# Optimization experiments

Hardware: AMD Instinct MI355X
Metric: run time of the kernel (lower is better)

## Reference

```python
import math
import jax, jax.numpy as jnp
import numpy as np

P_NEW = 10000  # module init: new=10000


def _design_filter(p_full=10000, q_full=48000, L=10, beta=5.0):
    """Octave-style anti-alias FIR: kaiser-windowed sinc, normalized to sum 1
    (the module stores window = h / sum(h))."""
    g = math.gcd(p_full, q_full)
    p, q = p_full // g, q_full // g          # 5, 24
    order = 2 * L * max(p, q)                # 480 -> 481 taps (odd)
    t = np.arange(-order // 2, order // 2 + 1)
    cutoff = 1.0 / (2 * max(p, q))           # normalized cycles/sample
    h = 2 * cutoff * np.sinc(2 * cutoff * t) * np.kaiser(order + 1, beta)
    h = h / np.sum(h)
    return h.astype(np.float32)


def setup_inputs() -> dict:
    key = jax.random.key(0)
    B, T = 32, 1440000  # 32 channels, 30 s @ 48 kHz
    x = jax.random.normal(key, (B, T), dtype=jnp.float32)
    h = jnp.asarray(_design_filter())  # [481]
    return {"x": x, "h": h, "orig_fs": 48000}


def reference(x, h, orig_fs):
    # resample_poly: upsample by `up` (zero-insert), FIR filter, decimate by `down`
    up, down = P_NEW, int(orig_fs)
    g = math.gcd(up, down)
    up //= g
    down //= g                                   # 5, 24 for 48 kHz
    if up == 1 and down == 1:
        return x

    half_len = (h.shape[0] - 1) // 2
    h = h * up                                   # gain compensation
    n_in = x.shape[-1]

    n_pre_pad = (down - half_len % down) % down
    h_padded = jnp.pad(h, (n_pre_pad, 0))
    filt_len = h_padded.shape[0]
    h_flipped = jnp.flip(h_padded)[None, None, :]  # OIH

    x_flat = x.reshape(-1, 1, n_in)                # NCH
    # lhs_dilation=up == zero-stuffed upsample; torch pads filt_len-1 both sides
    # and the torch x_up carries (up-1) trailing zeros -> extra right pad.
    # window_strides=down == the y[..., ::down] decimation, computed without waste.
    y_down = jax.lax.conv_general_dilated(
        x_flat, h_flipped,
        window_strides=(down,),
        padding=[(filt_len - 1, filt_len - 1 + up - 1)],
        lhs_dilation=(up,),
        dimension_numbers=("NCH", "OIH", "NCH"),
    )

    n_out = n_in * up // down + (1 if (n_in * up) % down else 0)
    n_pre_remove = (half_len + n_pre_pad) // down
    y = y_down[..., n_pre_remove:n_pre_remove + n_out]
    return y.reshape(x.shape[:-1] + (n_out,))
```

## Files before the change

### kernel.cpp

```cpp
#include <hip/hip_runtime.h>


#define NIN    1440000
#define NOUTR  300000
#define NROWS  32
#define KTOT   60000
#define NCHUNK 938
#define S      8
#define NBX    118
#define TILE_E 1632
#define TILE_P 1648
#define NV4    408

typedef __attribute__((ext_vector_type(8))) short short8v;
typedef __attribute__((ext_vector_type(4))) float float4v;

__device__ __forceinline__ unsigned short f2b(float f) {
    unsigned u = __builtin_bit_cast(unsigned, f);
    u += 0x7fff + ((u >> 16) & 1);
    return (unsigned short)(u >> 16);
}

__global__ void prep_taps_kernel(const float* __restrict__ h,
                                 unsigned short* __restrict__ Bpk) {
    int i = blockIdx.x * blockDim.x + threadIdx.x;
    if (i < 2048) {
        int j = i & 7, l = (i >> 3) & 63, m = i >> 9;
        int d = l & 15, q = l >> 4;
        int c = 32 * m + 8 * q + j;
        int t = 24 * d + 480 - 5 * c;
        float v = (d < 5 && t >= 0 && t <= 480) ? h[t] * 5.0f : 0.0f;
        Bpk[i] = f2b(v);
    }
}

__global__ __launch_bounds__(256, 6) void resample_kernel(
    const float* __restrict__ x, const unsigned short* __restrict__ Bpk,
    float* __restrict__ y)
{
    __shared__ short ldsb[TILE_P];
    const int tid  = threadIdx.x;
    const int lane = tid & 63;
    const int wv   = tid >> 6;
    const int row  = blockIdx.y;
    const int cb   = blockIdx.x * S;
    const float* __restrict__ xr = x + (size_t)row * NIN;

    short8v B0 = *reinterpret_cast<const short8v*>(Bpk + (0 * 64 + lane) * 8);
    short8v B1 = *reinterpret_cast<const short8v*>(Bpk + (1 * 64 + lane) * 8);
    short8v B2 = *reinterpret_cast<const short8v*>(Bpk + (2 * 64 + lane) * 8);
    short8v B3 = *reinterpret_cast<const short8v*>(Bpk + (3 * 64 + lane) * 8);

    if (tid < TILE_P - TILE_E) ldsb[TILE_E + tid] = 0;

    auto stc = [&](int i4, float4 v) {
        unsigned lo = (unsigned)f2b(v.x) | ((unsigned)f2b(v.y) << 16);
        unsigned hi = (unsigned)f2b(v.z) | ((unsigned)f2b(v.w) << 16);
        *reinterpret_cast<uint2*>(&ldsb[4 * i4]) = make_uint2(lo, hi);
    };

    for (int s = 0; s < S; ++s) {
        const int ct = cb + s;
        if (ct >= NCHUNK) break;
        const long g0 = 1536L * ct - 48;

        __syncthreads();
        if (g0 >= 0 && g0 + TILE_E <= NIN) {
            const float4* __restrict__ p = reinterpret_cast<const float4*>(xr + g0);
            stc(tid, p[tid]);
            if (tid < NV4 - 256) stc(tid + 256, p[tid + 256]);
        } else {
            auto ld = [&](int i4) {
                float v[4];
                #pragma unroll
                for (int j = 0; j < 4; ++j) {
                    const long g = g0 + 4L * i4 + j;
                    v[j] = (g >= 0 && g < NIN) ? xr[g] : 0.0f;
                }
                stc(i4, make_float4(v[0], v[1], v[2], v[3]));
            };
            ld(tid);
            if (tid < NV4 - 256) ld(tid + 256);
        }
        __syncthreads();

        const int r = lane & 15, q = lane >> 4;
        const short* __restrict__ ap = &ldsb[24 * (16 * wv + r) + 8 * q];
        const short8v A0 = *reinterpret_cast<const short8v*>(ap);
        const short8v A1 = *reinterpret_cast<const short8v*>(ap + 32);
        const short8v A2 = *reinterpret_cast<const short8v*>(ap + 64);
        const short8v A3 = *reinterpret_cast<const short8v*>(ap + 96);

        float4v acc = {0.f, 0.f, 0.f, 0.f};
        acc = __builtin_amdgcn_mfma_f32_16x16x32_bf16(A0, B0, acc, 0, 0, 0);
        acc = __builtin_amdgcn_mfma_f32_16x16x32_bf16(A1, B1, acc, 0, 0, 0);
        acc = __builtin_amdgcn_mfma_f32_16x16x32_bf16(A2, B2, acc, 0, 0, 0);
        acc = __builtin_amdgcn_mfma_f32_16x16x32_bf16(A3, B3, acc, 0, 0, 0);

        const int d = lane & 15;
        if (d < 5) {
            const int kbase = 64 * ct + 16 * wv + 4 * q;
            float* __restrict__ yr = y + (size_t)row * NOUTR;
            #pragma unroll
            for (int j = 0; j < 4; ++j) {
                const int k = kbase + j;
                if (k < KTOT) yr[5 * (size_t)k + d] = acc[j];
            }
        }
    }
}

extern "C" void kernel_launch(void* const* d_in, const int* in_sizes, int n_in,
                              void* d_out, int out_size, void* d_ws, size_t ws_size,
                              hipStream_t stream) {
    const float* x = (const float*)d_in[0];
    const float* h = (const float*)d_in[1];
    float* y = (float*)d_out;
    unsigned short* Bpk = (unsigned short*)d_ws;

    prep_taps_kernel<<<8, 256, 0, stream>>>(h, Bpk);
    dim3 grid(NBX, NROWS);
    resample_kernel<<<grid, 256, 0, stream>>>(x, Bpk, y);
}
```

Measured before the change: 43.51 us.

## Double-buffer LDS tiles and prefetch next chunk into registers during MFMA

Adds a second LDS buffer so the next chunk's global loads are issued into registers before the current chunk's MFMA work and are written to the alternate buffer afterwards. This removes one barrier per iteration and hides global load latency behind compute and stores. Loading also moves to 8 floats per thread on 204 threads, packing to bf16 with the hardware v_cvt_pk_bf16_f32 instruction instead of the manual rounding. Occupancy hint rises from 6 to 7 blocks. Risks are more register pressure and idle threads during loading.

New measurement: 44.05 us. About the same (+1.2%).

```diff
diff --git a/kernel.cpp b/kernel.cpp
--- a/kernel.cpp
+++ b/kernel.cpp
@@ -10,7 +10,7 @@
 #define NBX    118
 #define TILE_E 1632
 #define TILE_P 1648
-#define NV4    408
+#define NT8    204
 
 typedef __attribute__((ext_vector_type(8))) short short8v;
 typedef __attribute__((ext_vector_type(4))) float float4v;
@@ -34,58 +34,71 @@
     }
 }
 
-__global__ __launch_bounds__(256, 6) void resample_kernel(
+__global__ __launch_bounds__(256, 7) void resample_kernel(
     const float* __restrict__ x, const unsigned short* __restrict__ Bpk,
     float* __restrict__ y)
 {
-    __shared__ short ldsb[TILE_P];
+    __shared__ short ldsb[2][TILE_P];
     const int tid  = threadIdx.x;
     const int lane = tid & 63;
     const int wv   = tid >> 6;
     const int row  = blockIdx.y;
     const int cb   = blockIdx.x * S;
+    const int n    = min(S, NCHUNK - cb);
     const float* __restrict__ xr = x + (size_t)row * NIN;
 
-    short8v B0 = *reinterpret_cast<const short8v*>(Bpk + (0 * 64 + lane) * 8);
-    short8v B1 = *reinterpret_cast<const short8v*>(Bpk + (1 * 64 + lane) * 8);
-    short8v B2 = *reinterpret_cast<const short8v*>(Bpk + (2 * 64 + lane) * 8);
-    short8v B3 = *reinterpret_cast<const short8v*>(Bpk + (3 * 64 + lane) * 8);
+    const short8v B0 = *reinterpret_cast<const short8v*>(Bpk + (0 * 64 + lane) * 8);
+    const short8v B1 = *reinterpret_cast<const short8v*>(Bpk + (1 * 64 + lane) * 8);
+    const short8v B2 = *reinterpret_cast<const short8v*>(Bpk + (2 * 64 + lane) * 8);
+    const short8v B3 = *reinterpret_cast<const short8v*>(Bpk + (3 * 64 + lane) * 8);
 
-    if (tid < TILE_P - TILE_E) ldsb[TILE_E + tid] = 0;
+    if (tid < 16) {
+        ldsb[0][TILE_E + tid] = 0;
+        ldsb[1][TILE_E + tid] = 0;
+    }
 
-    auto stc = [&](int i4, float4 v) {
-        unsigned lo = (unsigned)f2b(v.x) | ((unsigned)f2b(v.y) << 16);
-        unsigned hi = (unsigned)f2b(v.z) | ((unsigned)f2b(v.w) << 16);
-        *reinterpret_cast<uint2*>(&ldsb[4 * i4]) = make_uint2(lo, hi);
+    float4 pa, pb;
+
+    auto load_regs = [&](int c) {
+        const int g0 = 1536 * c - 48;
+        if (tid < NT8) {
+            if (g0 >= 0 && g0 + TILE_E <= NIN) {
+                const float4* __restrict__ p = reinterpret_cast<const float4*>(xr + g0);
+                pa = p[2 * tid];
+                pb = p[2 * tid + 1];
+            } else {
+                float v[8];
+                #pragma unroll
+                for (int j = 0; j < 8; ++j) {
+                    const int g = g0 + 8 * tid + j;
+                    v[j] = ((unsigned)g < NIN) ? xr[g] : 0.0f;
+                }
+                pa = make_float4(v[0], v[1], v[2], v[3]);
+                pb = make_float4(v[4], v[5], v[6], v[7]);
+            }
+        }
     };
 
-    for (int s = 0; s < S; ++s) {
-        const int ct = cb + s;
-        if (ct >= NCHUNK) break;
-        const long g0 = 1536L * ct - 48;
+    auto write_buf = [&](int b) {
+        if (tid < NT8) {
+            unsigned r0, r1, r2, r3;
+            asm("v_cvt_pk_bf16_f32 %0, %1, %2" : "=v"(r0) : "v"(pa.x), "v"(pa.y));
+            asm("v_cvt_pk_bf16_f32 %0, %1, %2" : "=v"(r1) : "v"(pa.z), "v"(pa.w));
+            asm("v_cvt_pk_bf16_f32 %0, %1, %2" : "=v"(r2) : "v"(pb.x), "v"(pb.y));
+            asm("v_cvt_pk_bf16_f32 %0, %1, %2" : "=v"(r3) : "v"(pb.z), "v"(pb.w));
+            *reinterpret_cast<uint4*>(&ldsb[b][8 * tid]) = make_uint4(r0, r1, r2, r3);
+        }
+    };
 
-        __syncthreads();
-        if (g0 >= 0 && g0 + TILE_E <= NIN) {
-            const float4* __restrict__ p = reinterpret_cast<const float4*>(xr + g0);
-            stc(tid, p[tid]);
-            if (tid < NV4 - 256) stc(tid + 256, p[tid + 256]);
-        } else {
-            auto ld = [&](int i4) {
-                float v[4];
-                #pragma unroll
-                for (int j = 0; j < 4; ++j) {
-                    const long g = g0 + 4L * i4 + j;
-                    v[j] = (g >= 0 && g < NIN) ? xr[g] : 0.0f;
-                }
-                stc(i4, make_float4(v[0], v[1], v[2], v[3]));
-            };
-            ld(tid);
-            if (tid < NV4 - 256) ld(tid + 256);
-        }
-        __syncthreads();
+    load_regs(cb);
+    write_buf(0);
+    __syncthreads();
+
+    for (int s = 0; s < n; ++s) {
+        if (s + 1 < n) load_regs(cb + s + 1);
 
         const int r = lane & 15, q = lane >> 4;
-        const short* __restrict__ ap = &ldsb[24 * (16 * wv + r) + 8 * q];
+        const short* __restrict__ ap = &ldsb[s & 1][24 * (16 * wv + r) + 8 * q];
         const short8v A0 = *reinterpret_cast<const short8v*>(ap);
         const short8v A1 = *reinterpret_cast<const short8v*>(ap + 32);
         const short8v A2 = *reinterpret_cast<const short8v*>(ap + 64);
@@ -99,7 +112,7 @@
 
         const int d = lane & 15;
         if (d < 5) {
-            const int kbase = 64 * ct + 16 * wv + 4 * q;
+            const int kbase = 64 * (cb + s) + 16 * wv + 4 * q;
             float* __restrict__ yr = y + (size_t)row * NOUTR;
             #pragma unroll
             for (int j = 0; j < 4; ++j) {
@@ -107,6 +120,9 @@
                 if (k < KTOT) yr[5 * (size_t)k + d] = acc[j];
             }
         }
+
+        if (s + 1 < n) write_buf((s + 1) & 1);
+        __syncthreads();
     }
 }
 
```

## Load MFMA A-fragments directly from global memory, dropping LDS staging and barriers

Applied to the files above, without the earlier changes.

Each lane now reads its own overlapping input window straight from global memory into registers and converts it to bf16 with the packed convert instruction, instead of staging the tile through shared memory behind two barriers per chunk. Chunks per block are halved so the grid doubles, and the occupancy hint rises from 6 to 7. This removes LDS traffic and synchronisation but makes each input element be read by several lanes (about 2.5x redundant global/L2 reads), relying on caches to absorb it.

After: 55.85 us. +28.4%, slower.

```diff
diff --git a/kernel.cpp b/kernel.cpp
--- a/kernel.cpp
+++ b/kernel.cpp
@@ -6,11 +6,9 @@
 #define NROWS  32
 #define KTOT   60000
 #define NCHUNK 938
-#define S      8
-#define NBX    118
-#define TILE_E 1632
-#define TILE_P 1648
-#define NV4    408
+#define S      4
+#define NBX    235
+#define TAPN   600
 
 typedef __attribute__((ext_vector_type(8))) short short8v;
 typedef __attribute__((ext_vector_type(4))) float float4v;
@@ -34,11 +32,19 @@
     }
 }
 
-__global__ __launch_bounds__(256, 6) void resample_kernel(
+__device__ __forceinline__ short8v pack_frag(const float4& a, const float4& b) {
+    unsigned r0, r1, r2, r3;
+    asm("v_cvt_pk_bf16_f32 %0, %1, %2" : "=v"(r0) : "v"(a.x), "v"(a.y));
+    asm("v_cvt_pk_bf16_f32 %0, %1, %2" : "=v"(r1) : "v"(a.z), "v"(a.w));
+    asm("v_cvt_pk_bf16_f32 %0, %1, %2" : "=v"(r2) : "v"(b.x), "v"(b.y));
+    asm("v_cvt_pk_bf16_f32 %0, %1, %2" : "=v"(r3) : "v"(b.z), "v"(b.w));
+    return __builtin_bit_cast(short8v, make_uint4(r0, r1, r2, r3));
+}
+
+__global__ __launch_bounds__(256, 7) void resample_kernel(
     const float* __restrict__ x, const unsigned short* __restrict__ Bpk,
     float* __restrict__ y)
 {
-    __shared__ short ldsb[TILE_P];
     const int tid  = threadIdx.x;
     const int lane = tid & 63;
     const int wv   = tid >> 6;
@@ -46,50 +52,48 @@
     const int cb   = blockIdx.x * S;
     const float* __restrict__ xr = x + (size_t)row * NIN;
 
-    short8v B0 = *reinterpret_cast<const short8v*>(Bpk + (0 * 64 + lane) * 8);
-    short8v B1 = *reinterpret_cast<const short8v*>(Bpk + (1 * 64 + lane) * 8);
-    short8v B2 = *reinterpret_cast<const short8v*>(Bpk + (2 * 64 + lane) * 8);
-    short8v B3 = *reinterpret_cast<const short8v*>(Bpk + (3 * 64 + lane) * 8);
+    const short8v B0 = *reinterpret_cast<const short8v*>(Bpk + (0 * 64 + lane) * 8);
+    const short8v B1 = *reinterpret_cast<const short8v*>(Bpk + (1 * 64 + lane) * 8);
+    const short8v B2 = *reinterpret_cast<const short8v*>(Bpk + (2 * 64 + lane) * 8);
+    const short8v B3 = *reinterpret_cast<const short8v*>(Bpk + (3 * 64 + lane) * 8);
 
-    if (tid < TILE_P - TILE_E) ldsb[TILE_E + tid] = 0;
-
-    auto stc = [&](int i4, float4 v) {
-        unsigned lo = (unsigned)f2b(v.x) | ((unsigned)f2b(v.y) << 16);
-        unsigned hi = (unsigned)f2b(v.z) | ((unsigned)f2b(v.w) << 16);
-        *reinterpret_cast<uint2*>(&ldsb[4 * i4]) = make_uint2(lo, hi);
-    };
+    const int r = lane & 15, q = lane >> 4;
+    const int loff = 24 * (16 * wv + r) + 8 * q;
 
     for (int s = 0; s < S; ++s) {
         const int ct = cb + s;
         if (ct >= NCHUNK) break;
-        const long g0 = 1536L * ct - 48;
+        const int g0 = 1536 * ct - 48;
+        const int gl = g0 + loff;
 
-        __syncthreads();
-        if (g0 >= 0 && g0 + TILE_E <= NIN) {
-            const float4* __restrict__ p = reinterpret_cast<const float4*>(xr + g0);
-            stc(tid, p[tid]);
-            if (tid < NV4 - 256) stc(tid + 256, p[tid + 256]);
+        float4 p0, p1, p2, p3, p4, p5, p6, p7;
+        if (g0 >= 0 && g0 + 1632 <= NIN) {
+            const float4* __restrict__ p = reinterpret_cast<const float4*>(xr + gl);
+            p0 = p[0]; p1 = p[1];
+            p2 = p[8]; p3 = p[9];
+            p4 = p[16]; p5 = p[17];
+            p6 = p[24]; p7 = p[25];
         } else {
-            auto ld = [&](int i4) {
-                float v[4];
+            auto ld8 = [&](int base, float4& a, float4& b) {
+                float v[8];
                 #pragma unroll
-                for (int j = 0; j < 4; ++j) {
-                    const long g = g0 + 4L * i4 + j;
-                    v[j] = (g >= 0 && g < NIN) ? xr[g] : 0.0f;
+                for (int j = 0; j < 8; ++j) {
+                    const int g = base + j;
+                    v[j] = ((unsigned)g < NIN) ? xr[g] : 0.0f;
                 }
-                stc(i4, make_float4(v[0], v[1], v[2], v[3]));
+                a = make_float4(v[0], v[1], v[2], v[3]);
+                b = make_float4(v[4], v[5], v[6], v[7]);
             };
-            ld(tid);
-            if (tid < NV4 - 256) ld(tid + 256);
+            ld8(gl,      p0, p1);
+            ld8(gl + 32, p2, p3);
+            ld8(gl + 64, p4, p5);
+            ld8(gl + 96, p6, p7);
         }
-        __syncthreads();
 
-        const int r = lane & 15, q = lane >> 4;
-        const short* __restrict__ ap = &ldsb[24 * (16 * wv + r) + 8 * q];
-        const short8v A0 = *reinterpret_cast<const short8v*>(ap);
-        const short8v A1 = *reinterpret_cast<const short8v*>(ap + 32);
-        const short8v A2 = *reinterpret_cast<const short8v*>(ap + 64);
-        const short8v A3 = *reinterpret_cast<const short8v*>(ap + 96);
+        const short8v A0 = pack_frag(p0, p1);
+        const short8v A1 = pack_frag(p2, p3);
+        const short8v A2 = pack_frag(p4, p5);
+        const short8v A3 = pack_frag(p6, p7);
 
         float4v acc = {0.f, 0.f, 0.f, 0.f};
         acc = __builtin_amdgcn_mfma_f32_16x16x32_bf16(A0, B0, acc, 0, 0, 0);
```
